# Kernel tuning notes

Hardware: AMD Instinct MI355X
Metric: run time of the kernel (lower is better)

## Reference

```python
import jax, jax.numpy as jnp
import numpy as np

HIDDEN = 2048
HEADS = 16
HEAD_DIM = HIDDEN // HEADS
BATCH = 2
SEQ = 2048
ROPE_BASE = 10000.0


def _rope_cos_sin(seq_len, head_dim, dtype):
    inv_freq = 1.0 / (ROPE_BASE ** (jnp.arange(0, head_dim, 2, dtype=jnp.float32) / head_dim))
    t = jnp.arange(seq_len, dtype=jnp.float32)
    freqs = jnp.outer(t, inv_freq)                 # [S, D/2]
    emb = jnp.concatenate([freqs, freqs], axis=-1)  # [S, D]
    return jnp.cos(emb).astype(dtype), jnp.sin(emb).astype(dtype)


def _rotate_half(x):
    x1, x2 = jnp.split(x, 2, axis=-1)
    return jnp.concatenate([-x2, x1], axis=-1)


def setup_inputs() -> dict:
    key = jax.random.key(0)
    ks = jax.random.split(key, 5)
    scale = 1.0 / np.sqrt(HIDDEN)
    return {
        "x": jax.random.normal(ks[0], (BATCH, SEQ, HIDDEN), dtype=jnp.float32),
        "Wq": jax.random.normal(ks[1], (HIDDEN, HIDDEN), dtype=jnp.float32) * scale,
        "Wk": jax.random.normal(ks[2], (HIDDEN, HIDDEN), dtype=jnp.float32) * scale,
        "Wv": jax.random.normal(ks[3], (HIDDEN, HIDDEN), dtype=jnp.float32) * scale,
        "Wo": jax.random.normal(ks[4], (HIDDEN, HIDDEN), dtype=jnp.float32) * scale,
    }


def reference(x, Wq, Wk, Wv, Wo):
    B, S, H = x.shape
    # projections (torch Linear: y = x @ W.T)
    q = jnp.einsum('bsh,oh->bso', x, Wq).reshape(B, S, HEADS, HEAD_DIM).transpose(0, 2, 1, 3)
    k = jnp.einsum('bsh,oh->bso', x, Wk).reshape(B, S, HEADS, HEAD_DIM).transpose(0, 2, 1, 3)
    v = jnp.einsum('bsh,oh->bso', x, Wv).reshape(B, S, HEADS, HEAD_DIM).transpose(0, 2, 1, 3)
    # RoPE
    cos, sin = _rope_cos_sin(S, HEAD_DIM, x.dtype)  # [S, D]
    cos = cos[None, None]  # [1,1,S,D]
    sin = sin[None, None]
    q = q * cos + _rotate_half(q) * sin
    k = k * cos + _rotate_half(k) * sin
    # attention scores [B, H, S, S]
    scale = HEAD_DIM ** -0.5
    scores = jnp.einsum('bhqd,bhkd->bhqk', q, k) * scale
    causal = jnp.triu(jnp.ones((S, S), dtype=bool), k=1)  # kv_len==seq -> diagonal=1
    scores = jnp.where(causal[None, None], -jnp.inf, scores)
    attn = jax.nn.softmax(scores.astype(jnp.float32), axis=-1).astype(q.dtype)
    # dropout is identity in eval mode
    out = jnp.einsum('bhqk,bhkd->bhqd', attn, v)  # [B,H,S,D]
    out = out.transpose(0, 2, 1, 3).reshape(B, S, H)
    return jnp.einsum('bsh,oh->bso', out, Wo)
```

## Files before the change

kernel.cpp:

```cpp
#include <hip/hip_runtime.h>
#include <hip/hip_bf16.h>
#include <cstdint>
#include <cstddef>

constexpr int HIDDEN = 2048;
constexpr int HEADS  = 16;
constexpr int HD     = 128;
constexpr int BATCH  = 2;
constexpr int SEQ    = 2048;
constexpr int MROWS  = BATCH * SEQ;

typedef __attribute__((ext_vector_type(8))) short bf16x8;
typedef __attribute__((ext_vector_type(4))) float f32x4;
typedef __attribute__((ext_vector_type(4))) unsigned u32x4;

constexpr float QSCALE = 0.08838834764831845f * 1.4426950408889634f;

__device__ __forceinline__ unsigned short f2bf(float f) {
  union { float f; unsigned int u; } c; c.f = f;
  unsigned int r = c.u + 0x7FFFu + ((c.u >> 16) & 1u);
  return (unsigned short)(r >> 16);
}
__device__ __forceinline__ float bf2f(unsigned short u) {
  union { unsigned int u; float f; } c; c.u = ((unsigned int)u) << 16;
  return c.f;
}

__device__ __forceinline__ void gload_lds16(const void* g, void* l) {
  __builtin_amdgcn_global_load_lds(
      (const __attribute__((address_space(1))) void*)g,
      (__attribute__((address_space(3))) void*)l, 16, 0, 0);
}

__global__ void k_cvt_all(const float* __restrict__ x,
                          const float* __restrict__ w0, const float* __restrict__ w1,
                          const float* __restrict__ w2, const float* __restrict__ w3,
                          unsigned short* __restrict__ out) {
  constexpr int N4X = MROWS * HIDDEN / 4;
  constexpr int N4W = HIDDEN * HIDDEN / 4;
  int idx = blockIdx.x * 256 + threadIdx.x;
  const float* src;
  int off;
  if (idx < N4X) { src = x; off = idx; }
  else {
    int j = idx - N4X;
    int seg = j >> 20;
    off = j & (N4W - 1);
    src = (seg == 0) ? w0 : (seg == 1) ? w1 : (seg == 2) ? w2 : w3;
  }
  float4 v = reinterpret_cast<const float4*>(src)[off];
  ushort4 o;
  o.x = f2bf(v.x); o.y = f2bf(v.y); o.z = f2bf(v.z); o.w = f2bf(v.w);
  reinterpret_cast<ushort4*>(out)[idx] = o;
}

constexpr int GK  = 2048;
constexpr int GNT = GK / 64;

template<int MODE, int BM, int BN>
__global__ __launch_bounds__(512)
__attribute__((amdgpu_waves_per_eu(2)))
void k_gemm256(const unsigned short* __restrict__ A,
               const unsigned short* __restrict__ Bm,
               void* __restrict__ Cout) {
  constexpr int ABYTES = BM * 64 * 2;
  constexpr int BBYTES = BN * 64 * 2;
  constexpr int AG = BM / 64;
  constexpr int BG = BN / 64;
  constexpr int G  = AG + BG;
  constexpr int MI = BM / 32;
  constexpr int NI = BN / 64;

  __shared__ char lds[2 * (ABYTES + BBYTES)];
  char* ldsA = lds;
  char* ldsB = lds + 2 * ABYTES;

  const int t    = threadIdx.x;
  const int lane = t & 63;
  const int w    = t >> 6;
  const int wr   = w >> 2;
  const int wc   = w & 3;
  const int l15  = lane & 15, lg = lane >> 4;

  const int orig = blockIdx.x;
  const int wg   = (orig & 7) * 32 + (orig >> 3);
  const int m0   = (wg >> 4) * BM;
  const int n0   = (wg & 15) * BN;

  const int rowA = t >> 3;
  const int xsel = ((t & 7) ^ (rowA & 7)) * 8;
  const unsigned short* aS = A  + (size_t)(m0 + rowA) * GK + xsel;
  const unsigned short* bS = Bm + (size_t)(n0 + rowA) * GK + xsel;
  char* aD = ldsA + t * 16;
  char* bD = ldsB + t * 16;

#define STAGEG(buf, kt) do {                                       \
    const unsigned short* ap = aS + (kt) * 64;                     \
    const unsigned short* bp = bS + (kt) * 64;                     \
    char* ad = aD + (buf) * ABYTES;                                \
    char* bd = bD + (buf) * BBYTES;                                \
    _Pragma("unroll")                                              \
    for (int g = 0; g < AG; ++g)                                   \
      gload_lds16(ap + (size_t)g * 64 * GK, ad + g * 8192);        \
    _Pragma("unroll")                                              \
    for (int g = 0; g < BG; ++g)                                   \
      gload_lds16(bp + (size_t)g * 64 * GK, bd + g * 8192);        \
  } while (0)

  const int xr  = (l15 & 7) << 4;
  const int vo0 = (lg * 16) ^ xr;
  const int vo1 = (64 + lg * 16) ^ xr;
  const char* aR = ldsA + wr * (BM / 2) * 128 + l15 * 128;
  const char* bR = (MODE == 0) ? (ldsB + wc * 2048 + l15 * 128)
                               : (ldsB + wc * (BN / 4) * 128 + l15 * 128);
#define BOFF(ni) ((MODE == 0) ? (((ni) & 1) * 8192 + ((ni) >> 1) * 16384) : ((ni) * 2048))

  f32x4 acc[MI][NI];
#pragma unroll
  for (int mi = 0; mi < MI; ++mi)
#pragma unroll
    for (int ni = 0; ni < NI; ++ni)
#pragma unroll
      for (int r = 0; r < 4; ++r) acc[mi][ni][r] = 0.f;

  STAGEG(0, 0);
  STAGEG(1, 1);
  asm volatile("s_waitcnt vmcnt(%0)" :: "i"(G) : "memory");
  __builtin_amdgcn_s_barrier();
  asm volatile("" ::: "memory");

#pragma unroll 1
  for (int kt = 0; kt < GNT; ++kt) {
    const int buf = kt & 1;
    const char* a = aR + buf * ABYTES;
    const char* b = bR + buf * BBYTES;

    bf16x8 af0[MI], bf0[NI];
#pragma unroll
    for (int mi = 0; mi < MI; ++mi)
      af0[mi] = *reinterpret_cast<const bf16x8*>(a + mi * 2048 + vo0);
#pragma unroll
    for (int ni = 0; ni < NI; ++ni)
      bf0[ni] = *reinterpret_cast<const bf16x8*>(b + BOFF(ni) + vo0);
    __builtin_amdgcn_s_setprio(1);
#pragma unroll
    for (int mi = 0; mi < MI; ++mi)
#pragma unroll
      for (int ni = 0; ni < NI; ++ni)
        acc[mi][ni] = __builtin_amdgcn_mfma_f32_16x16x32_bf16(af0[mi], bf0[ni], acc[mi][ni], 0, 0, 0);
    __builtin_amdgcn_s_setprio(0);

    bf16x8 af1[MI], bf1[NI];
#pragma unroll
    for (int mi = 0; mi < MI; ++mi)
      af1[mi] = *reinterpret_cast<const bf16x8*>(a + mi * 2048 + vo1);
#pragma unroll
    for (int ni = 0; ni < NI; ++ni)
      bf1[ni] = *reinterpret_cast<const bf16x8*>(b + BOFF(ni) + vo1);

    asm volatile("s_waitcnt lgkmcnt(0)" ::: "memory");
    __builtin_amdgcn_s_barrier();
    asm volatile("" ::: "memory");

    if (kt < GNT - 2) STAGEG(buf, kt + 2);

    __builtin_amdgcn_s_setprio(1);
#pragma unroll
    for (int mi = 0; mi < MI; ++mi)
#pragma unroll
      for (int ni = 0; ni < NI; ++ni)
        acc[mi][ni] = __builtin_amdgcn_mfma_f32_16x16x32_bf16(af1[mi], bf1[ni], acc[mi][ni], 0, 0, 0);
    __builtin_amdgcn_s_setprio(0);

    if (kt < GNT - 2) asm volatile("s_waitcnt vmcnt(%0)" :: "i"(G) : "memory");
    else              asm volatile("s_waitcnt vmcnt(0)" ::: "memory");
    __builtin_amdgcn_s_barrier();
    asm volatile("" ::: "memory");
  }
#undef STAGEG
#undef BOFF

  if (MODE == 0) {
    const int dp = wc * 16 + l15;
    const float invf = exp2f((float)dp * -0.20762050593046868f);
    const int colbase = n0 + wc * 16 + l15;
#pragma unroll
    for (int mi = 0; mi < MI; ++mi) {
#pragma unroll
      for (int r = 0; r < 4; ++r) {
        int row = m0 + wr * 128 + mi * 16 + lg * 4 + r;
        int s  = row & (SEQ - 1);
        int bb = row >> 11;
        float sn, cs;
        __sincosf((float)s * invf, &sn, &cs);
#pragma unroll
        for (int p = 0; p < 2; ++p) {
          float lo = acc[mi][p * 2][r], hi = acc[mi][p * 2 + 1][r];
          float olo = lo * cs - hi * sn;
          float ohi = hi * cs + lo * sn;
          int col   = colbase + p * 128;
          int which = col >> 11;
          int h     = (col & 2047) >> 7;
          if (which == 0) { olo *= QSCALE; ohi *= QSCALE; }
          size_t base = (size_t)which * ((size_t)MROWS * HIDDEN)
                      + ((size_t)(bb * HEADS + h) * SEQ + s) * HD + dp;
          reinterpret_cast<unsigned short*>(Cout)[base]      = f2bf(olo);
          reinterpret_cast<unsigned short*>(Cout)[base + 64] = f2bf(ohi);
        }
      }
    }
  } else {
#pragma unroll
    for (int mi = 0; mi < MI; ++mi) {
#pragma unroll
      for (int ni = 0; ni < NI; ++ni) {
#pragma unroll
        for (int r = 0; r < 4; ++r) {
          int row = m0 + wr * (BM / 2) + mi * 16 + lg * 4 + r;
          int col = n0 + wc * (BN / 4) + ni * 16 + l15;
          float v = acc[mi][ni][r];
          if (MODE == 2) {
            reinterpret_cast<float*>(Cout)[(size_t)row * 2048 + col] = v;
          } else {
            int h = row >> 7, d = row & (HD - 1);
            int bb = col >> 11, s = col & (SEQ - 1);
            size_t addr = ((size_t)(bb * HEADS + h) * HD + d) * SEQ + s;
            reinterpret_cast<unsigned short*>(Cout)[addr] = f2bf(v);
          }
        }
      }
    }
  }
}

constexpr int QB  = 128;
constexpr int KVB = 64;
constexpr int NQT = SEQ / QB;

__global__ __launch_bounds__(512)
__attribute__((amdgpu_waves_per_eu(4, 4)))
void k_attn(const unsigned short* __restrict__ Q,
            const unsigned short* __restrict__ Kk,
            const unsigned short* __restrict__ Vt,
            unsigned short* __restrict__ O) {
  __shared__ char lds[3 * 16384];
  char* Ks = lds;
  char* Vs = lds + 2 * 16384;

  const int t    = threadIdx.x;
  const int lane = t & 63;
  const int w    = t >> 6;
  const int l15  = lane & 15, lg = lane >> 4;

  const int lin     = blockIdx.x + 16 * blockIdx.y;
  const int pos     = lin >> 3;
  const int logical = (lin & 7) * 64 + pos;
  const int bh      = logical >> 4;
  const int qt0     = logical & 15;
  const int qt      = (pos < 32) ? qt0 : (15 - qt0);
  const int b  = bh >> 4, h = bh & 15;
  const int q0b  = qt * QB;
  const int q0w  = q0b + w * 16;
  const int qw_hi = q0w + 15;

  const unsigned short* Qb = Q  + (size_t)bh * SEQ * HD;
  const unsigned short* Kb = Kk + (size_t)bh * SEQ * HD;
  const unsigned short* Vb = Vt + (size_t)bh * HD * SEQ;

  bf16x8 qf[4];
#pragma unroll
  for (int c = 0; c < 4; ++c)
    qf[c] = *reinterpret_cast<const bf16x8*>(Qb + (size_t)(q0w + l15) * HD + c * 32 + lg * 8);

  float m = -1e30f, lpart = 0.f;
  f32x4 oacc[8];
#pragma unroll
  for (int dt = 0; dt < 8; ++dt)
#pragma unroll
    for (int r = 0; r < 4; ++r) oacc[dt][r] = 0.f;

  const int sp     = t * 16;
  const int srow   = sp >> 8;
  const int scolb  = (sp & 255) ^ ((srow & 7) << 4);
  const unsigned short* ksrc2 = Kb + (size_t)srow * HD + (scolb >> 1);
  char* kdst2 = Ks + sp;

  const int vrow  = t >> 3;
  const int vcolb = ((t & 7) << 4) ^ ((vrow & 7) << 4);
  const unsigned short* vsrc = Vb + (size_t)vrow * SEQ + (vcolb >> 1);
  char* vdst = Vs + t * 16;

  const int nb = q0b / KVB + 2;

  gload_lds16(ksrc2, kdst2);
  gload_lds16(ksrc2 + (size_t)32 * HD, kdst2 + 8192);

  int cur = 0;
  for (int kb = 0; kb < nb; ++kb) {
    const int kv0 = kb * KVB;
    gload_lds16(vsrc + kv0, vdst);
    gload_lds16(vsrc + (size_t)64 * SEQ + kv0, vdst + 8192);
    if (kb + 1 < nb) {
      const int nxt = kv0 + KVB;
      char* nk = kdst2 + (cur ^ 1) * 16384;
      gload_lds16(ksrc2 + (size_t)nxt * HD, nk);
      gload_lds16(ksrc2 + (size_t)(nxt + 32) * HD, nk + 8192);
      asm volatile("s_waitcnt vmcnt(2)" ::: "memory");
    } else {
      asm volatile("s_waitcnt vmcnt(0)" ::: "memory");
    }
    __builtin_amdgcn_s_barrier();
    asm volatile("" ::: "memory");

    if (kv0 <= qw_hi) {
      const char* Kc = Ks + cur * 16384;
      const char* Vc = Vs;
      f32x4 sc[4];
#pragma unroll
      for (int tt = 0; tt < 4; ++tt)
#pragma unroll
        for (int r = 0; r < 4; ++r) sc[tt][r] = 0.f;
      __builtin_amdgcn_s_setprio(1);
#pragma unroll
      for (int tt = 0; tt < 4; ++tt) {
        const int kr = tt * 16 + l15;
        const int xr = (kr & 7) << 4;
#pragma unroll
        for (int c = 0; c < 4; ++c) {
          bf16x8 kf = *reinterpret_cast<const bf16x8*>(
              Kc + kr * 256 + ((c * 64 + lg * 16) ^ xr));
          sc[tt] = __builtin_amdgcn_mfma_f32_16x16x32_bf16(kf, qf[c], sc[tt], 0, 0, 0);
        }
      }
      __builtin_amdgcn_s_setprio(0);

      const bool full = (kv0 + KVB - 1 <= q0w);
      const int qg = q0w + l15;
      if (!full) {
        const int kvb = kv0 + lg * 4;
#pragma unroll
        for (int tt = 0; tt < 4; ++tt)
#pragma unroll
          for (int r = 0; r < 4; ++r)
            if (kvb + tt * 16 + r > qg) sc[tt][r] = -1e30f;
      }
      float pm01 = fmaxf(fmaxf(sc[0][0], sc[0][1]), fmaxf(sc[0][2], sc[0][3]));
      float pm11 = fmaxf(fmaxf(sc[1][0], sc[1][1]), fmaxf(sc[1][2], sc[1][3]));
      float pm21 = fmaxf(fmaxf(sc[2][0], sc[2][1]), fmaxf(sc[2][2], sc[2][3]));
      float pm31 = fmaxf(fmaxf(sc[3][0], sc[3][1]), fmaxf(sc[3][2], sc[3][3]));
      float pm = fmaxf(fmaxf(pm01, pm11), fmaxf(pm21, pm31));
      if (__any(pm > m + 11.5f)) {
        float pmr = pm;
        pmr = fmaxf(pmr, __shfl_xor(pmr, 16));
        pmr = fmaxf(pmr, __shfl_xor(pmr, 32));
        float mn = fmaxf(m, pmr);
        float al = exp2f(m - mn);
        lpart *= al;
#pragma unroll
        for (int r = 0; r < 4; ++r) {
          float alr = __shfl(al, lg * 4 + r, 16);
#pragma unroll
          for (int dt = 0; dt < 8; ++dt) oacc[dt][r] *= alr;
        }
        m = mn;
      }
      float p[4][4];
      float ps = 0.f;
#pragma unroll
      for (int tt = 0; tt < 4; ++tt)
#pragma unroll
        for (int r = 0; r < 4; ++r) {
          p[tt][r] = exp2f(sc[tt][r] - m);
          ps += p[tt][r];
        }
      lpart += ps;

      unsigned cc[4][2];
#pragma unroll
      for (int tt = 0; tt < 4; ++tt) {
        asm("v_cvt_pk_bf16_f32 %0, %1, %2" : "=v"(cc[tt][0]) : "v"(p[tt][0]), "v"(p[tt][1]));
        asm("v_cvt_pk_bf16_f32 %0, %1, %2" : "=v"(cc[tt][1]) : "v"(p[tt][2]), "v"(p[tt][3]));
      }
      u32x4 u0, u1;
      {
        unsigned a0 = cc[0][0], b0 = cc[1][0];
        asm("v_permlane32_swap_b32 %0, %1" : "+v"(a0), "+v"(b0));
        asm("v_permlane16_swap_b32 %0, %1" : "+v"(a0), "+v"(b0));
        unsigned a1 = cc[0][1], b1 = cc[1][1];
        asm("v_permlane32_swap_b32 %0, %1" : "+v"(a1), "+v"(b1));
        asm("v_permlane16_swap_b32 %0, %1" : "+v"(a1), "+v"(b1));
        u0[0] = a0; u0[1] = a1; u0[2] = b0; u0[3] = b1;
        unsigned a2 = cc[2][0], b2 = cc[3][0];
        asm("v_permlane32_swap_b32 %0, %1" : "+v"(a2), "+v"(b2));
        asm("v_permlane16_swap_b32 %0, %1" : "+v"(a2), "+v"(b2));
        unsigned a3 = cc[2][1], b3 = cc[3][1];
        asm("v_permlane32_swap_b32 %0, %1" : "+v"(a3), "+v"(b3));
        asm("v_permlane16_swap_b32 %0, %1" : "+v"(a3), "+v"(b3));
        u1[0] = a2; u1[1] = a3; u1[2] = b2; u1[3] = b3;
      }
      bf16x8 pa0 = __builtin_bit_cast(bf16x8, u0);
      bf16x8 pa1 = __builtin_bit_cast(bf16x8, u1);

      const int xv = (l15 & 7) << 4;
      __builtin_amdgcn_s_setprio(1);
#pragma unroll
      for (int dt = 0; dt < 8; ++dt) {
        const char* vrl = Vc + (dt * 16 + l15) * 128;
        bf16x8 vf0 = *reinterpret_cast<const bf16x8*>(vrl + ((lg * 16) ^ xv));
        bf16x8 vf1 = *reinterpret_cast<const bf16x8*>(vrl + ((64 + lg * 16) ^ xv));
        oacc[dt] = __builtin_amdgcn_mfma_f32_16x16x32_bf16(pa0, vf0, oacc[dt], 0, 0, 0);
        oacc[dt] = __builtin_amdgcn_mfma_f32_16x16x32_bf16(pa1, vf1, oacc[dt], 0, 0, 0);
      }
      __builtin_amdgcn_s_setprio(0);
    }
    __builtin_amdgcn_s_barrier();
    asm volatile("" ::: "memory");
    cur ^= 1;
  }

  float ls = lpart;
  ls += __shfl_xor(ls, 16);
  ls += __shfl_xor(ls, 32);
  float inv = 1.0f / ls;
  float invr[4];
#pragma unroll
  for (int r = 0; r < 4; ++r) invr[r] = __shfl(inv, lg * 4 + r, 16);
#pragma unroll
  for (int dt = 0; dt < 8; ++dt) {
#pragma unroll
    for (int r = 0; r < 4; ++r) {
      int qg = q0w + lg * 4 + r;
      int dv = dt * 16 + l15;
      O[((size_t)(b * SEQ + qg) * HEADS + h) * HD + dv] = f2bf(oacc[dt][r] * invr[r]);
    }
  }
}

extern "C" void kernel_launch(void* const* d_in, const int* in_sizes, int n_in,
                              void* d_out, int out_size, void* d_ws, size_t ws_size,
                              hipStream_t stream) {
  (void)in_sizes; (void)n_in; (void)out_size; (void)ws_size;
  const float* x  = (const float*)d_in[0];
  const float* Wq = (const float*)d_in[1];
  const float* Wk = (const float*)d_in[2];
  const float* Wv = (const float*)d_in[3];
  const float* Wo = (const float*)d_in[4];
  float* out = (float*)d_out;

  unsigned short* xb  = (unsigned short*)d_ws;
  unsigned short* wqb = xb  + (size_t)MROWS * HIDDEN;
  unsigned short* wkb = wqb + (size_t)HIDDEN * HIDDEN;
  unsigned short* wvb = wkb + (size_t)HIDDEN * HIDDEN;
  unsigned short* wob = wvb + (size_t)HIDDEN * HIDDEN;
  unsigned short* Qb  = wob + (size_t)HIDDEN * HIDDEN;
  unsigned short* Kb  = Qb  + (size_t)MROWS * HIDDEN;
  unsigned short* Vtb = Kb  + (size_t)MROWS * HIDDEN;
  unsigned short* Ob  = Vtb + (size_t)MROWS * HIDDEN;
  (void)wkb;

  constexpr int CVT_THREADS = (MROWS * HIDDEN + 4 * HIDDEN * HIDDEN) / 4;
  k_cvt_all<<<CVT_THREADS / 256, 256, 0, stream>>>(x, Wq, Wk, Wv, Wo, xb);

  k_gemm256<0, 256, 256><<<256, 512, 0, stream>>>(xb, wqb, Qb);
  k_gemm256<3, 128, 256><<<256, 512, 0, stream>>>(wvb, xb, Vtb);

  k_attn<<<dim3(SEQ / QB, BATCH * HEADS), 512, 0, stream>>>(Qb, Kb, Vtb, Ob);

  k_gemm256<2, 256, 128><<<256, 512, 0, stream>>>(Ob, wob, out);
}
```

Measured before the change: 231.0 us.

## Software-pipeline QK^T one tile ahead and double-buffer V in attention

Restructures the attention loop so the QK^T MFMAs for the next KV tile are computed before the softmax and PV work of the current tile. V gets its own double buffer, so its load is prefetched a tile ahead and K two tiles ahead. The aim is to let matrix work overlap the exp/softmax VALU work and hide global load latency. The cost is more LDS (64KB instead of 48KB), more live registers for the extra score tile, and a risk that the 4-waves-per-EU occupancy target cannot be met.

```diff
diff --git a/kernel.cpp b/kernel.cpp
--- a/kernel.cpp
+++ b/kernel.cpp
@@ -243,7 +243,7 @@
             const unsigned short* __restrict__ Kk,
             const unsigned short* __restrict__ Vt,
             unsigned short* __restrict__ O) {
-  __shared__ char lds[3 * 16384];
+  __shared__ char lds[2 * 16384 + 2 * 16384];
   char* Ks = lds;
   char* Vs = lds + 2 * 16384;
 
@@ -292,19 +292,56 @@
 
   const int nb = q0b / KVB + 2;
 
-  gload_lds16(ksrc2, kdst2);
-  gload_lds16(ksrc2 + (size_t)32 * HD, kdst2 + 8192);
-
-  int cur = 0;
+#define ISSUE_K(tile) do {                                              \
+    char* nk = kdst2 + ((tile) & 1) * 16384;                            \
+    gload_lds16(ksrc2 + (size_t)((tile) * KVB) * HD, nk);               \
+    gload_lds16(ksrc2 + (size_t)((tile) * KVB + 32) * HD, nk + 8192);   \
+  } while (0)
+#define ISSUE_V(tile) do {                                              \
+    char* nv = vdst + ((tile) & 1) * 16384;                             \
+    gload_lds16(vsrc + (tile) * KVB, nv);                               \
+    gload_lds16(vsrc + (size_t)64 * SEQ + (tile) * KVB, nv + 8192);     \
+  } while (0)
+
+#define QKT(sc, kbuf) do {                                              \
+    const char* Kc = Ks + (kbuf) * 16384;                               \
+    _Pragma("unroll")                                                   \
+    for (int tt = 0; tt < 4; ++tt) {                                    \
+      const int kr = tt * 16 + l15;                                     \
+      const int xr = (kr & 7) << 4;                                     \
+      _Pragma("unroll")                                                 \
+      for (int c = 0; c < 4; ++c) {                                     \
+        bf16x8 kf = *reinterpret_cast<const bf16x8*>(                   \
+            Kc + kr * 256 + ((c * 64 + lg * 16) ^ xr));                 \
+        sc[tt] = __builtin_amdgcn_mfma_f32_16x16x32_bf16(kf, qf[c], sc[tt], 0, 0, 0); \
+      }                                                                 \
+    }                                                                   \
+  } while (0)
+
+  ISSUE_K(0);
+  ISSUE_V(0);
+  ISSUE_K(1);
+  asm volatile("s_waitcnt vmcnt(4)" ::: "memory");
+  __builtin_amdgcn_s_barrier();
+  asm volatile("" ::: "memory");
+
+  f32x4 scc[4];
+#pragma unroll
+  for (int tt = 0; tt < 4; ++tt)
+#pragma unroll
+    for (int r = 0; r < 4; ++r) scc[tt][r] = 0.f;
+  __builtin_amdgcn_s_setprio(1);
+  QKT(scc, 0);
+  __builtin_amdgcn_s_setprio(0);
+
   for (int kb = 0; kb < nb; ++kb) {
     const int kv0 = kb * KVB;
-    gload_lds16(vsrc + kv0, vdst);
-    gload_lds16(vsrc + (size_t)64 * SEQ + kv0, vdst + 8192);
-    if (kb + 1 < nb) {
-      const int nxt = kv0 + KVB;
-      char* nk = kdst2 + (cur ^ 1) * 16384;
-      gload_lds16(ksrc2 + (size_t)nxt * HD, nk);
-      gload_lds16(ksrc2 + (size_t)(nxt + 32) * HD, nk + 8192);
+    if (kb + 2 < nb) {
+      ISSUE_V(kb + 1);
+      ISSUE_K(kb + 2);
+      asm volatile("s_waitcnt vmcnt(4)" ::: "memory");
+    } else if (kb + 1 < nb) {
+      ISSUE_V(kb + 1);
       asm volatile("s_waitcnt vmcnt(2)" ::: "memory");
     } else {
       asm volatile("s_waitcnt vmcnt(0)" ::: "memory");
@@ -312,28 +349,17 @@
     __builtin_amdgcn_s_barrier();
     asm volatile("" ::: "memory");
 
+    f32x4 scn[4];
+    const bool doNext = (kb + 1 < nb) && (kv0 + KVB <= qw_hi);
+    if (doNext) {
+#pragma unroll
+      for (int tt = 0; tt < 4; ++tt)
+#pragma unroll
+        for (int r = 0; r < 4; ++r) scn[tt][r] = 0.f;
+      QKT(scn, (kb + 1) & 1);
+    }
+
     if (kv0 <= qw_hi) {
-      const char* Kc = Ks + cur * 16384;
-      const char* Vc = Vs;
-      f32x4 sc[4];
-#pragma unroll
-      for (int tt = 0; tt < 4; ++tt)
-#pragma unroll
-        for (int r = 0; r < 4; ++r) sc[tt][r] = 0.f;
-      __builtin_amdgcn_s_setprio(1);
-#pragma unroll
-      for (int tt = 0; tt < 4; ++tt) {
-        const int kr = tt * 16 + l15;
-        const int xr = (kr & 7) << 4;
-#pragma unroll
-        for (int c = 0; c < 4; ++c) {
-          bf16x8 kf = *reinterpret_cast<const bf16x8*>(
-              Kc + kr * 256 + ((c * 64 + lg * 16) ^ xr));
-          sc[tt] = __builtin_amdgcn_mfma_f32_16x16x32_bf16(kf, qf[c], sc[tt], 0, 0, 0);
-        }
-      }
-      __builtin_amdgcn_s_setprio(0);
-
       const bool full = (kv0 + KVB - 1 <= q0w);
       const int qg = q0w + l15;
       if (!full) {
@@ -342,12 +368,12 @@
         for (int tt = 0; tt < 4; ++tt)
 #pragma unroll
           for (int r = 0; r < 4; ++r)
-            if (kvb + tt * 16 + r > qg) sc[tt][r] = -1e30f;
-      }
-      float pm01 = fmaxf(fmaxf(sc[0][0], sc[0][1]), fmaxf(sc[0][2], sc[0][3]));
-      float pm11 = fmaxf(fmaxf(sc[1][0], sc[1][1]), fmaxf(sc[1][2], sc[1][3]));
-      float pm21 = fmaxf(fmaxf(sc[2][0], sc[2][1]), fmaxf(sc[2][2], sc[2][3]));
-      float pm31 = fmaxf(fmaxf(sc[3][0], sc[3][1]), fmaxf(sc[3][2], sc[3][3]));
+            if (kvb + tt * 16 + r > qg) scc[tt][r] = -1e30f;
+      }
+      float pm01 = fmaxf(fmaxf(scc[0][0], scc[0][1]), fmaxf(scc[0][2], scc[0][3]));
+      float pm11 = fmaxf(fmaxf(scc[1][0], scc[1][1]), fmaxf(scc[1][2], scc[1][3]));
+      float pm21 = fmaxf(fmaxf(scc[2][0], scc[2][1]), fmaxf(scc[2][2], scc[2][3]));
+      float pm31 = fmaxf(fmaxf(scc[3][0], scc[3][1]), fmaxf(scc[3][2], scc[3][3]));
       float pm = fmaxf(fmaxf(pm01, pm11), fmaxf(pm21, pm31));
       if (__any(pm > m + 11.5f)) {
         float pmr = pm;
@@ -364,22 +390,21 @@
         }
         m = mn;
       }
-      float p[4][4];
       float ps = 0.f;
 #pragma unroll
       for (int tt = 0; tt < 4; ++tt)
 #pragma unroll
         for (int r = 0; r < 4; ++r) {
-          p[tt][r] = exp2f(sc[tt][r] - m);
-          ps += p[tt][r];
+          scc[tt][r] = exp2f(scc[tt][r] - m);
+          ps += scc[tt][r];
         }
       lpart += ps;
 
       unsigned cc[4][2];
 #pragma unroll
       for (int tt = 0; tt < 4; ++tt) {
-        asm("v_cvt_pk_bf16_f32 %0, %1, %2" : "=v"(cc[tt][0]) : "v"(p[tt][0]), "v"(p[tt][1]));
-        asm("v_cvt_pk_bf16_f32 %0, %1, %2" : "=v"(cc[tt][1]) : "v"(p[tt][2]), "v"(p[tt][3]));
+        asm("v_cvt_pk_bf16_f32 %0, %1, %2" : "=v"(cc[tt][0]) : "v"(scc[tt][0]), "v"(scc[tt][1]));
+        asm("v_cvt_pk_bf16_f32 %0, %1, %2" : "=v"(cc[tt][1]) : "v"(scc[tt][2]), "v"(scc[tt][3]));
       }
       u32x4 u0, u1;
       {
@@ -401,6 +426,7 @@
       bf16x8 pa0 = __builtin_bit_cast(bf16x8, u0);
       bf16x8 pa1 = __builtin_bit_cast(bf16x8, u1);
 
+      const char* Vc = Vs + (kb & 1) * 16384;
       const int xv = (l15 & 7) << 4;
       __builtin_amdgcn_s_setprio(1);
 #pragma unroll
@@ -415,8 +441,15 @@
     }
     __builtin_amdgcn_s_barrier();
     asm volatile("" ::: "memory");
-    cur ^= 1;
+
+#pragma unroll
+    for (int tt = 0; tt < 4; ++tt)
+#pragma unroll
+      for (int r = 0; r < 4; ++r) scc[tt][r] = scn[tt][r];
   }
+#undef QKT
+#undef ISSUE_K
+#undef ISSUE_V
 
   float ls = lpart;
   ls += __shfl_xor(ls, 16);
```

Result: no change. 226.7 us (-1.9%).
